# Performance work log

Hardware: AMD Instinct MI355X
Metric: run time of the kernel (lower is better)

## Reference

```python
import jax, jax.numpy as jnp
import numpy as np

K = 1024
D = 64
BETA = 0.25
DECAY = 0.99
EPS = 1e-05


def setup_inputs() -> dict:
    key = jax.random.key(0)
    k1, k2 = jax.random.split(key)
    z = jax.random.normal(k1, (32, D, 64, 64), dtype=jnp.float32)
    # nn.init.uniform_(weight, -1/K, 1/K)
    embedding = jax.random.uniform(k2, (K, D), dtype=jnp.float32, minval=-1.0 / K, maxval=1.0 / K)
    # post-_maybe_init_ema_from_embedding state
    cluster_size = jnp.ones((K,), dtype=jnp.float32)
    embed_avg = embedding.copy()
    return {"z": z, "embedding": embedding, "cluster_size": cluster_size, "embed_avg": embed_avg}


def reference(z, embedding, cluster_size, embed_avg):
    B, C, H, W = z.shape
    z_nhwc = jnp.transpose(z, (0, 2, 3, 1))            # [B,H,W,D]
    flat = z_nhwc.reshape(-1, D)                        # [N,D]

    x2 = jnp.sum(flat * flat, axis=1, keepdims=True)    # [N,1]
    w2 = jnp.sum(embedding * embedding, axis=1)         # [K]
    dist = x2 + w2[None, :] - 2.0 * flat @ embedding.T  # [N,K]
    idx = jnp.argmin(dist, axis=1)                      # [N] int

    z_q = embedding[idx].reshape(z_nhwc.shape)          # gather

    # EMA codebook update (training, update=True)
    counts = jax.ops.segment_sum(jnp.ones_like(idx, dtype=jnp.float32), idx, num_segments=K)
    embed_sum = jax.ops.segment_sum(flat, idx, num_segments=K)  # [K,D]
    new_cluster_size = cluster_size * DECAY + (1.0 - DECAY) * counts
    new_embed_avg = embed_avg * DECAY + (1.0 - DECAY) * embed_sum
    n = jnp.sum(new_cluster_size)
    smoothed = (new_cluster_size + EPS) / (n + K * EPS) * n
    new_embedding = new_embed_avg / smoothed[:, None]

    # commitment loss (z_q detached) + straight-through estimator
    loss = BETA * jnp.mean((z_nhwc - jax.lax.stop_gradient(z_q)) ** 2)
    z_q_ste = z_nhwc + jax.lax.stop_gradient(z_q - z_nhwc)
    z_q_out = jnp.transpose(z_q_ste, (0, 3, 1, 2))      # back to [B,C,H,W]
    return (z_q_out, idx, loss, new_embedding, new_cluster_size, new_embed_avg)
```

## Files before the change

kernel.cpp:

```cpp
#include <hip/hip_runtime.h>
#include <hip/hip_bf16.h>

#define NROWS 131072
#define DDIM  64
#define KCODES 1024
#define HW    4096

#define OFF_ZQ   0ull
#define OFF_IDX  8388608ull
#define OFF_LOSS 8519680ull
#define OFF_EMB  8519681ull
#define OFF_NCS  8585217ull
#define OFF_EAVG 8586241ull

#define SCR_B0    34078724ull
#define SCR_WLO   (SCR_B0 + 131072ull)
#define SCR_W2O   (SCR_B0 + 262144ull)
#define LCAP      20480u

#define FWS_KSCR   16777216ull
#define FWS_ES     16777216ull
#define FWS_CNTF   17039360ull
#define FWS_SX2    17043456ull
#define FWS_SMOOTH 17047552ull
#define FWS_LIST   17301504ull
#define FWS_RMIN   17383424ull
#define FWS_CNTR   17547264ull
#define FWS_TOTAL  17547268ull

#define WSO_KSCR   262144ull
#define WSO_LOSSB  786432ull
#define WSO_SMOOTH 788480ull
#define WSO_CNT    792576ull
#define WSO_ESUM   858112ull

#define GAPTHR 8e-5f

typedef __attribute__((ext_vector_type(8))) short bf16x8;
typedef __attribute__((ext_vector_type(4))) float f32x4;

#define GLOAD_LDS16(gp, lp)                                                     \
    __builtin_amdgcn_global_load_lds(                                           \
        (const __attribute__((address_space(1))) void*)(gp),                    \
        (__attribute__((address_space(3))) void*)(lp), 16, 0, 0)

__device__ __forceinline__ float np_sumsq64(const float* v) {
#pragma clang fp contract(off)
    float r0 = v[0]*v[0], r1 = v[1]*v[1], r2 = v[2]*v[2], r3 = v[3]*v[3];
    float r4 = v[4]*v[4], r5 = v[5]*v[5], r6 = v[6]*v[6], r7 = v[7]*v[7];
    for (int i = 8; i < 64; i += 8) {
        r0 += v[i+0]*v[i+0]; r1 += v[i+1]*v[i+1];
        r2 += v[i+2]*v[i+2]; r3 += v[i+3]*v[i+3];
        r4 += v[i+4]*v[i+4]; r5 += v[i+5]*v[i+5];
        r6 += v[i+6]*v[i+6]; r7 += v[i+7]*v[i+7];
    }
    return ((r0+r1)+(r2+r3))+((r4+r5)+(r6+r7));
}
__device__ __forceinline__ float mul_rn(float a, float b) {
#pragma clang fp contract(off)
    return a * b;
}
__device__ __forceinline__ float add_rn(float a, float b) {
#pragma clang fp contract(off)
    return a + b;
}
__device__ __forceinline__ float sub2_rn(float s, float a) {
#pragma clang fp contract(off)
    return s - 2.0f * a;
}
__device__ __forceinline__ unsigned bf16rne(float v) {
    unsigned b = __float_as_uint(v);
    return (b + 0x7FFFu + ((b >> 16) & 1u)) >> 16;
}
__device__ __forceinline__ float bfu2f(unsigned short u) {
    return __uint_as_float(((unsigned)u) << 16);
}
__device__ __forceinline__ unsigned flipf(float v) {
    unsigned b = __float_as_uint(v);
    return b ^ (0x80000000u | (unsigned)((int)b >> 31));
}
__device__ __forceinline__ float unflip_val(unsigned u) {
    u &= 0xFFFFFC00u;
    unsigned mask = 0x80000000u | (unsigned)((int)(~u) >> 31);
    return __uint_as_float(u ^ mask);
}

__global__ __launch_bounds__(256) void prep_kernel(
        const float* __restrict__ emb, unsigned short* __restrict__ wh,
        unsigned short* __restrict__ wl, float* __restrict__ w2,
        float* __restrict__ embT) {
    __shared__ float tile[64][65];
    const int t = threadIdx.x;
    const int kb = blockIdx.x * 64;
#pragma unroll
    for (int i = 0; i < 16; ++i) {
        const int e = t + i * 256;
        const int kl = e >> 6, d = e & 63;
        const float v = emb[(size_t)(kb + kl) * DDIM + d];
        tile[kl][d] = v;
        const unsigned rh = bf16rne(v);
        const float lv = v - bfu2f((unsigned short)rh);
        wh[(size_t)(kb + kl) * DDIM + d] = (unsigned short)rh;
        wl[(size_t)(kb + kl) * DDIM + d] = (unsigned short)bf16rne(lv);
    }
    __syncthreads();
    if (t < 64) w2[kb + t] = np_sumsq64(&tile[t][0]);
#pragma unroll
    for (int i = 0; i < 16; ++i) {
        const int e = t + i * 256;
        const int d = e >> 6, kl = e & 63;
        embT[(size_t)d * KCODES + kb + kl] = tile[kl][d];
    }
}

#define CBLOAD(S, c)                                                          \
    { const size_t a_ = ((size_t)(((c) * 16 + col) * DDIM + grp * 8));        \
      wh##S##0 = *(const bf16x8*)(wh + a_);                                   \
      wh##S##1 = *(const bf16x8*)(wh + a_ + 32);                              \
      wl##S##0 = *(const bf16x8*)(wl + a_);                                   \
      wl##S##1 = *(const bf16x8*)(wl + a_ + 32); }

__global__ __launch_bounds__(512, 2) void score2_kernel(
        const float* __restrict__ z, const float* __restrict__ emb,
        const unsigned short* __restrict__ wh, const unsigned short* __restrict__ wl,
        const float* __restrict__ w2g, float* __restrict__ out,
        unsigned short* __restrict__ xT, unsigned* __restrict__ list,
        unsigned long long* __restrict__ rmin, unsigned* __restrict__ counter) {
    __shared__ __attribute__((aligned(16))) unsigned short sxt[64][512];
    __shared__ __attribute__((aligned(16))) unsigned short cb[2][2][4][512];
    __shared__ unsigned k1s[512];

    const int tid = threadIdx.x;
    const int lane = tid & 63, wid = tid >> 6;
    const int col = lane & 15, grp = lane >> 4;
    const int nb = blockIdx.x * 512;
    const int b = nb >> 12, hb = (nb >> 6) & 63;
    const int w4 = (tid & 15) * 4, h8 = (tid >> 4) & 7, dg = tid >> 7;

    {
#pragma unroll
        for (int j = 0; j < 16; ++j) {
            const int d = dg * 16 + j;
            const float4 v = *(const float4*)&z[((size_t)(b * 64 + d)) * HW + (hb + h8) * 64 + w4];
            ushort4 u;
            u.x = (unsigned short)bf16rne(v.x);
            u.y = (unsigned short)bf16rne(v.y);
            u.z = (unsigned short)bf16rne(v.z);
            u.w = (unsigned short)bf16rne(v.w);
            *(ushort4*)&sxt[d][h8 * 64 + w4] = u;
        }
    }
    __syncthreads();

    bf16x8 fx[4][2];
#pragma unroll
    for (int rt = 0; rt < 4; ++rt)
#pragma unroll
        for (int kh = 0; kh < 2; ++kh) {
            const int row = wid * 64 + rt * 16 + col;
            bf16x8 f;
#pragma unroll
            for (int j = 0; j < 8; ++j)
                f[j] = (short)sxt[kh * 32 + grp * 8 + j][row];
            fx[rt][kh] = f;
            *(bf16x8*)&xT[(size_t)(nb + row) * DDIM + kh * 32 + grp * 8] = f;
        }

    const int pr = wid >> 2, sW = (wid >> 1) & 1, khW = wid & 1;
    const unsigned short* gsrc = (pr ? wl : wh) + khW * 32 + grp * 8
                               + (size_t)(sW * 16 + col) * DDIM;

    GLOAD_LDS16(gsrc, &cb[0][pr][sW * 2 + khW][0]);
    asm volatile("s_waitcnt vmcnt(0)" ::: "memory");
    __builtin_amdgcn_s_barrier();

    unsigned m1[4] = {~0u, ~0u, ~0u, ~0u}, m2[4] = {~0u, ~0u, ~0u, ~0u};

    for (int rd = 0; rd < 32; ++rd) {
        const int cur = rd & 1;
        if (rd < 31)
            GLOAD_LDS16(gsrc + (size_t)(rd + 1) * 32 * DDIM,
                        &cb[cur ^ 1][pr][sW * 2 + khW][0]);
#pragma unroll
        for (int s = 0; s < 2; ++s) {
            const bf16x8 vh0 = *(const bf16x8*)&cb[cur][0][s * 2 + 0][lane * 8];
            const bf16x8 vh1 = *(const bf16x8*)&cb[cur][0][s * 2 + 1][lane * 8];
            const bf16x8 vl0 = *(const bf16x8*)&cb[cur][1][s * 2 + 0][lane * 8];
            const bf16x8 vl1 = *(const bf16x8*)&cb[cur][1][s * 2 + 1][lane * 8];
            const int c = rd * 2 + s;
            const float4 w2v = *(const float4*)&w2g[c * 16 + grp * 4];
            const float* w2p = (const float*)&w2v;
#pragma unroll
            for (int rt = 0; rt < 4; ++rt) {
                f32x4 aA = {0.f, 0.f, 0.f, 0.f}, aB = {0.f, 0.f, 0.f, 0.f};
                aA = __builtin_amdgcn_mfma_f32_16x16x32_bf16(vh0, fx[rt][0], aA, 0, 0, 0);
                aA = __builtin_amdgcn_mfma_f32_16x16x32_bf16(vl0, fx[rt][0], aA, 0, 0, 0);
                aB = __builtin_amdgcn_mfma_f32_16x16x32_bf16(vh1, fx[rt][1], aB, 0, 0, 0);
                aB = __builtin_amdgcn_mfma_f32_16x16x32_bf16(vl1, fx[rt][1], aB, 0, 0, 0);
#pragma unroll
                for (int r = 0; r < 4; ++r) {
                    const float val = fmaf(-2.f, aA[r] + aB[r], w2p[r]);
                    const unsigned u = (flipf(val) & 0xFFFFFC00u) |
                                       (unsigned)(c * 16 + grp * 4 + r);
                    const unsigned mx = m1[rt] > u ? m1[rt] : u;
                    m1[rt] = m1[rt] < u ? m1[rt] : u;
                    m2[rt] = m2[rt] < mx ? m2[rt] : mx;
                }
            }
        }
        asm volatile("s_waitcnt vmcnt(0) lgkmcnt(0)" ::: "memory");
        __builtin_amdgcn_s_barrier();
    }

#pragma unroll
    for (int rt = 0; rt < 4; ++rt) {
        for (int off = 16; off <= 32; off <<= 1) {
            const unsigned o1 = (unsigned)__shfl_xor((int)m1[rt], off, 64);
            const unsigned o2 = (unsigned)__shfl_xor((int)m2[rt], off, 64);
            const unsigned mx = m1[rt] > o1 ? m1[rt] : o1;
            m1[rt] = m1[rt] < o1 ? m1[rt] : o1;
            const unsigned t2 = m2[rt] < o2 ? m2[rt] : o2;
            m2[rt] = t2 < mx ? t2 : mx;
        }
    }

    bool flag[4];
    unsigned long long mrt[4];
    unsigned wavecnt = 0;
#pragma unroll
    for (int rt = 0; rt < 4; ++rt) {
        flag[rt] = (grp == 0) &&
                   ((unflip_val(m2[rt]) - unflip_val(m1[rt])) < GAPTHR);
        mrt[rt] = __ballot(flag[rt]);
        wavecnt += (unsigned)__popcll(mrt[rt]);
    }

    if (grp == 0) {
#pragma unroll
        for (int rt = 0; rt < 4; ++rt) {
            const unsigned k = m1[rt] & 1023u;
            out[OFF_IDX + (size_t)(nb + wid * 64 + rt * 16 + col)] = (float)k;
            k1s[wid * 64 + rt * 16 + col] = k;
        }
    }

    unsigned base = 0;
    if (lane == 0 && wavecnt) base = atomicAdd(counter, wavecnt);
    base = (unsigned)__shfl((int)base, 0, 64);
    unsigned offrt = 0;
#pragma unroll
    for (int rt = 0; rt < 4; ++rt) {
        if (flag[rt]) {
            const unsigned offin =
                (unsigned)__popcll(mrt[rt] & ((lane == 0) ? 0ull : (~0ull >> (64 - lane))));
            const unsigned slot = base + offrt + offin;
            if (slot < LCAP) {
                list[slot] = (unsigned)(nb + wid * 64 + rt * 16 + col);
                rmin[slot] = ~0ull;
            }
        }
        offrt += (unsigned)__popcll(mrt[rt]);
    }

    __syncthreads();
    {
        const int r0 = h8 * 64 + w4;
        const float* e0 = emb + (size_t)k1s[r0 + 0] * DDIM;
        const float* e1 = emb + (size_t)k1s[r0 + 1] * DDIM;
        const float* e2 = emb + (size_t)k1s[r0 + 2] * DDIM;
        const float* e3 = emb + (size_t)k1s[r0 + 3] * DDIM;
#pragma unroll
        for (int j = 0; j < 16; ++j) {
            const int d = dg * 16 + j;
            float4 q;
            q.x = e0[d]; q.y = e1[d]; q.z = e2[d]; q.w = e3[d];
            *(float4*)&out[((size_t)(b * 64 + d)) * HW + (hb + h8) * 64 + w4] = q;
        }
    }
}

__global__ __launch_bounds__(256, 1) void rescanb_kernel(
        const float* __restrict__ z, const float* __restrict__ emb,
        const float* __restrict__ w2, const unsigned* __restrict__ list,
        const unsigned* __restrict__ counter,
        unsigned long long* __restrict__ rmin) {
    const int lane = threadIdx.x & 63;
    const int wid = __builtin_amdgcn_readfirstlane(threadIdx.x >> 6);
    unsigned cnt = __builtin_amdgcn_readfirstlane(*counter);
    if (cnt > LCAP) cnt = LCAP;
    if (cnt == 0) return;
    const unsigned W = ((cnt + 63) >> 6) * 8;

    for (unsigned w = blockIdx.x * 4 + wid; w < W; w += gridDim.x * 4) {
        const unsigned g = w >> 3, p = w & 7;
        const unsigned slot = g * 64 + lane;
        const bool valid = slot < cnt;
        const unsigned n = list[valid ? slot : 0];
        const unsigned hw = n & 4095u, bb = n >> 12;

        float x[64];
#pragma unroll
        for (int d = 0; d < 64; ++d)
            x[d] = z[(size_t)(bb * 64 + d) * (size_t)HW + hw];

        float r[8];
#pragma unroll
        for (int j = 0; j < 8; ++j) r[j] = mul_rn(x[j], x[j]);
#pragma unroll
        for (int i = 8; i < 64; i += 8)
#pragma unroll
            for (int j = 0; j < 8; ++j)
                r[j] = add_rn(r[j], mul_rn(x[i + j], x[i + j]));
        const float x2 = add_rn(add_rn(add_rn(r[0], r[1]), add_rn(r[2], r[3])),
                                add_rn(add_rn(r[4], r[5]), add_rn(r[6], r[7])));

        unsigned long long best = ~0ull;
        const int k0 = (int)p * 128;
        for (int k = k0; k < k0 + 128; k += 2) {
            const float* wa = emb + (size_t)k * DDIM;
            const float* wb = wa + DDIM;
            float aa = 0.f, ab = 0.f;
#pragma unroll
            for (int d = 0; d < 64; ++d) {
                aa = fmaf(x[d], wa[d], aa);
                ab = fmaf(x[d], wb[d], ab);
            }
            const float da = sub2_rn(add_rn(x2, w2[k]),     aa);
            const float db = sub2_rn(add_rn(x2, w2[k + 1]), ab);
            const unsigned long long ua =
                ((unsigned long long)flipf(da) << 10) | (unsigned long long)k;
            const unsigned long long ub =
                ((unsigned long long)flipf(db) << 10) | (unsigned long long)(k + 1);
            best = best < ua ? best : ua;
            best = best < ub ? best : ub;
        }
        if (valid) atomicMin(&rmin[slot], best);
    }
}

__global__ __launch_bounds__(256) void fix_kernel(
        const unsigned* __restrict__ list, const unsigned long long* __restrict__ rmin,
        const unsigned* __restrict__ counter, const float* __restrict__ emb,
        float* __restrict__ out) {
    unsigned cnt = *counter;
    if (cnt > LCAP) cnt = LCAP;
    const int lane = threadIdx.x & 63, ws = threadIdx.x >> 6;
    const unsigned t = blockIdx.x * 4 + ws;
    if (t >= cnt) return;
    const unsigned long long u = rmin[t];
    if (u == ~0ull) return;
    const unsigned k = (unsigned)(u & 1023ull);
    const unsigned n = list[t];
    if (lane == 0) out[OFF_IDX + (size_t)n] = (float)k;
    const unsigned hw = n & 4095u, bb = n >> 12;
    out[((size_t)(bb * 64 + lane)) * HW + hw] = emb[(size_t)k * DDIM + lane];
}

__global__ __launch_bounds__(256) void gather_kernel(
        const float* __restrict__ idxf, const unsigned short* __restrict__ xT,
        float* __restrict__ es, float* __restrict__ cntf, float* __restrict__ sx2a) {
    const int k = blockIdx.x;
    const int lane = threadIdx.x & 63, wid = threadIdx.x >> 6;
    const float fk = (float)k;
    float acc = 0.f, s2 = 0.f;
    unsigned cnt = 0;
    const int wbase = wid * 32768;

    float4 cur = *(const float4*)&idxf[wbase + lane * 4];
    for (int it = 0; it < 128; ++it) {
        float4 nxt;
        if (it + 1 < 128)
            nxt = *(const float4*)&idxf[wbase + (it + 1) * 256 + lane * 4];
        const float* cp = (const float*)&cur;
#pragma unroll
        for (int j = 0; j < 4; ++j) {
            unsigned long long m = __ballot(cp[j] == fk);
            cnt += (unsigned)__popcll(m);
            while (m) {
                const int src = __ffsll(m) - 1;
                m &= m - 1;
                const int n = wbase + it * 256 + src * 4 + j;
                const float xv = bfu2f(xT[(size_t)n * DDIM + lane]);
                acc += xv;
                s2 = fmaf(xv, xv, s2);
            }
        }
        cur = nxt;
    }
#pragma unroll
    for (int off = 32; off > 0; off >>= 1) s2 += __shfl_down(s2, off, 64);
    __shared__ float sacc[4][64];
    __shared__ float ssx2[4];
    __shared__ unsigned scnt[4];
    sacc[wid][lane] = acc;
    if (lane == 0) { ssx2[wid] = s2; scnt[wid] = cnt; }
    __syncthreads();
    if (wid == 0) {
        const float t = sacc[0][lane] + sacc[1][lane] + sacc[2][lane] + sacc[3][lane];
        es[(size_t)k * DDIM + lane] = t;
        if (lane == 0) {
            cntf[k] = (float)(scnt[0] + scnt[1] + scnt[2] + scnt[3]);
            sx2a[k] = ssx2[0] + ssx2[1] + ssx2[2] + ssx2[3];
        }
    }
}

__global__ __launch_bounds__(1024) void fin1_f(
        const float* __restrict__ cs, const float* __restrict__ emb,
        float* __restrict__ out, const float* __restrict__ w2,
        const float* __restrict__ es, const float* __restrict__ cntf,
        const float* __restrict__ sx2a, float* __restrict__ smoothed) {
    const int k = threadIdx.x;
    const float cnt = cntf[k];
    const float w2k = w2[k];
    const float* ek = es + (size_t)k * DDIM;
    const float* wk = emb + (size_t)k * DDIM;
    float dt = 0.f;
#pragma unroll
    for (int d = 0; d < DDIM; ++d) dt = fmaf(ek[d], wk[d], dt);
    const float lp = sx2a[k] - 2.f * dt + cnt * w2k;
    const float ncs = fmaf(0.01f, cnt, 0.99f * cs[k]);

    __shared__ float red[1024];
    red[k] = ncs;
    __syncthreads();
    for (int s = 512; s > 0; s >>= 1) {
        if (k < s) red[k] += red[k + s];
        __syncthreads();
    }
    const float nn = red[0];
    __syncthreads();
    red[k] = lp;
    __syncthreads();
    for (int s = 512; s > 0; s >>= 1) {
        if (k < s) red[k] += red[k + s];
        __syncthreads();
    }
    smoothed[k] = (ncs + 1e-5f) / (nn + 1024.f * 1e-5f) * nn;
    out[OFF_NCS + (size_t)k] = ncs;
    if (k == 0) out[OFF_LOSS] = 0.25f * red[0] / 8388608.f;
}

__global__ __launch_bounds__(256) void fin2_f(
        const float* __restrict__ eavg, float* __restrict__ out,
        const float* __restrict__ es, const float* __restrict__ smoothed) {
    const int e = blockIdx.x * 256 + threadIdx.x;
    const float ea = fmaf(0.01f, es[e], 0.99f * eavg[e]);
    out[OFF_EAVG + (size_t)e] = ea;
    out[OFF_EMB  + (size_t)e] = ea / smoothed[e >> 6];
}


#define CBCOMP(S, c)                                                          \
    { const float4 w2v = *(const float4*)&w2s[(c) * 16 + grp * 4];            \
      const float* w2p = (const float*)&w2v;                                  \
      _Pragma("unroll")                                                       \
      for (int rt = 0; rt < 2; ++rt) {                                        \
        f32x4 aA = {0.f,0.f,0.f,0.f}, aB = {0.f,0.f,0.f,0.f};                 \
        aA = __builtin_amdgcn_mfma_f32_16x16x32_bf16(wh##S##0, fx[rt][0], aA, 0, 0, 0); \
        aA = __builtin_amdgcn_mfma_f32_16x16x32_bf16(wl##S##0, fx[rt][0], aA, 0, 0, 0); \
        aB = __builtin_amdgcn_mfma_f32_16x16x32_bf16(wh##S##1, fx[rt][1], aB, 0, 0, 0); \
        aB = __builtin_amdgcn_mfma_f32_16x16x32_bf16(wl##S##1, fx[rt][1], aB, 0, 0, 0); \
        _Pragma("unroll")                                                     \
        for (int r = 0; r < 4; ++r) {                                         \
          const float val = fmaf(-2.f, aA[r] + aB[r], w2p[r]);                \
          const unsigned u = (flipf(val) & 0xFFFFFC00u) |                     \
                             (unsigned)((c) * 16 + grp * 4 + r);              \
          const unsigned mx = m1[rt] > u ? m1[rt] : u;                        \
          m1[rt] = m1[rt] < u ? m1[rt] : u;                                   \
          m2[rt] = m2[rt] < mx ? m2[rt] : mx;                                 \
        } } }

__global__ __launch_bounds__(512, 4) void score_kernel(
        const float* __restrict__ z,
        const unsigned short* __restrict__ wh, const unsigned short* __restrict__ wl,
        const float* __restrict__ w2, unsigned* __restrict__ kscr) {
    __shared__ __attribute__((aligned(16))) unsigned short sxt[64][260];
    __shared__ float w2s[KCODES];

    const int tid = threadIdx.x;
    const int lane = tid & 63, wid = tid >> 6;
    const int col = lane & 15, grp = lane >> 4;
    const int nb = blockIdx.x * 256;
    const int b = nb >> 12, hb = (nb >> 6) & 63;

    for (int i = tid; i < KCODES; i += 512) w2s[i] = w2[i];
    {
        const int h = lane >> 4, w4 = (lane & 15) * 4;
        const int row = h * 64 + w4;
#pragma unroll
        for (int it = 0; it < 8; ++it) {
            const int d = wid + 8 * it;
            const float4 v = *(const float4*)&z[((size_t)(b * 64 + d)) * HW + (hb + h) * 64 + w4];
            ushort4 u;
            u.x = (unsigned short)bf16rne(v.x);
            u.y = (unsigned short)bf16rne(v.y);
            u.z = (unsigned short)bf16rne(v.z);
            u.w = (unsigned short)bf16rne(v.w);
            *(ushort4*)&sxt[d][row] = u;
        }
    }
    __syncthreads();

    bf16x8 fx[2][2];
#pragma unroll
    for (int rt = 0; rt < 2; ++rt)
#pragma unroll
        for (int kh = 0; kh < 2; ++kh) {
            const int row = wid * 32 + rt * 16 + col;
            bf16x8 f;
#pragma unroll
            for (int j = 0; j < 8; ++j)
                f[j] = (short)sxt[kh * 32 + grp * 8 + j][row];
            fx[rt][kh] = f;
        }

    unsigned m1[2] = {~0u, ~0u}, m2[2] = {~0u, ~0u};
    bf16x8 whA0, whA1, wlA0, wlA1, whB0, whB1, wlB0, wlB1;

    CBLOAD(A, 0)
    for (int c = 0; c < 64; c += 2) {
        CBLOAD(B, c + 1)
        CBCOMP(A, c)
        if (c + 2 < 64) CBLOAD(A, c + 2)
        CBCOMP(B, c + 1)
    }
#pragma unroll
    for (int rt = 0; rt < 2; ++rt) {
        for (int off = 16; off <= 32; off <<= 1) {
            const unsigned o1 = (unsigned)__shfl_xor((int)m1[rt], off, 64);
            const unsigned o2 = (unsigned)__shfl_xor((int)m2[rt], off, 64);
            const unsigned mx = m1[rt] > o1 ? m1[rt] : o1;
            m1[rt] = m1[rt] < o1 ? m1[rt] : o1;
            const unsigned t2 = m2[rt] < o2 ? m2[rt] : o2;
            m2[rt] = t2 < mx ? t2 : mx;
        }
        if (grp == 0) {
            const bool fl = (unflip_val(m2[rt]) - unflip_val(m1[rt])) < GAPTHR;
            kscr[nb + wid * 32 + rt * 16 + col] =
                (m1[rt] & 1023u) | (fl ? 0x80000000u : 0u);
        }
    }
}

__global__ __launch_bounds__(512, 4) void output_kernel(
        const float* __restrict__ z, const float* __restrict__ emb,
        const float* __restrict__ embT, const float* __restrict__ w2,
        float* __restrict__ out, const unsigned* __restrict__ kscr,
        float* __restrict__ esum_p, unsigned* __restrict__ cnt_p,
        float* __restrict__ lossb, int pmask) {
    __shared__ __attribute__((aligned(16))) unsigned short sxt[64][260];
    __shared__ unsigned k1s[256];
    __shared__ float redl[8];

    const int tid = threadIdx.x;
    const int lane = tid & 63, wid = tid >> 6;
    const int nb = blockIdx.x * 256;
    const int b = nb >> 12, hb = (nb >> 6) & 63;

    {
        const int h = lane >> 4, w4 = (lane & 15) * 4;
        const int row = h * 64 + w4;
#pragma unroll
        for (int it = 0; it < 8; ++it) {
            const int d = wid + 8 * it;
            const float4 v = *(const float4*)&z[((size_t)(b * 64 + d)) * HW + (hb + h) * 64 + w4];
            ushort4 u;
            u.x = (unsigned short)bf16rne(v.x);
            u.y = (unsigned short)bf16rne(v.y);
            u.z = (unsigned short)bf16rne(v.z);
            u.w = (unsigned short)bf16rne(v.w);
            *(ushort4*)&sxt[d][row] = u;
        }
    }

    unsigned kf = 0;
    if (lane < 32) kf = kscr[nb + wid * 32 + lane];
    int k1 = (int)(kf & 1023u);
    unsigned long long need = __ballot((lane < 32) && (kf & 0x80000000u));
    while (need) {
        const int src = __ffsll(need) - 1;
        need &= need - 1;
        const int nr = nb + wid * 32 + src;
        const int wq = nr & 63, hq = (nr >> 6) & 63, bq = nr >> 12;
        const float xv = z[(size_t)bq * DDIM * HW + (size_t)lane * HW + hq * 64 + wq];
        const float p = mul_rn(xv, xv);
        float r = 0.f;
        for (int i = 0; i < 8; ++i) {
            const float t = __shfl(p, (i << 3) + (lane & 7), 64);
            r = add_rn(r, t);
        }
        const float s01 = add_rn(r, __shfl_xor(r, 1, 64));
        const float s03 = add_rn(s01, __shfl_xor(s01, 2, 64));
        const float s07 = add_rn(s03, __shfl_xor(s03, 4, 64));
        const float x2s = __shfl(s07, 0, 64);

        float acc[16];
#pragma unroll
        for (int j = 0; j < 16; ++j) acc[j] = 0.f;
        for (int d = 0; d < DDIM; ++d) {
            const float xd = __shfl(xv, d, 64);
            const float* ecol = embT + (size_t)d * KCODES + lane;
#pragma unroll
            for (int j = 0; j < 16; ++j)
                acc[j] = fmaf(ecol[64 * j], xd, acc[j]);
        }
        float bv = 1e30f;
        int bk = KCODES;
#pragma unroll
        for (int j = 0; j < 16; ++j) {
            const int kk = lane + 64 * j;
            const float s  = add_rn(x2s, w2[kk]);
            const float dv = sub2_rn(s, acc[j]);
            if (dv < bv) { bv = dv; bk = kk; }
        }
        for (int off = 32; off > 0; off >>= 1) {
            const float ov = __shfl_xor(bv, off, 64);
            const int   ok = __shfl_xor(bk, off, 64);
            if (ov < bv || (ov == bv && ok < bk)) { bv = ov; bk = ok; }
        }
        if (lane == src) k1 = bk;
    }
    if (lane < 32) k1s[wid * 32 + lane] = (unsigned)k1;
    __syncthreads();

    const int part = blockIdx.x & pmask;
    if (tid < 256) {
        const unsigned myk = k1s[tid];
        out[OFF_IDX + (size_t)(nb + tid)] = (float)myk;
        atomicAdd(&cnt_p[part * KCODES + myk], 1u);
    }

    float ls = 0.f;
    {
        const int h = lane >> 4, w4 = (lane & 15) * 4;
        const int row = h * 64 + w4;
#pragma unroll 2
        for (int it = 0; it < 8; ++it) {
            const int d = wid + 8 * it;
            float4 q;
            float* qp = (float*)&q;
#pragma unroll
            for (int j = 0; j < 4; ++j) {
                const unsigned k = k1s[row + j];
                const float wv = emb[(size_t)k * DDIM + d];
                qp[j] = wv;
                const float diff = bfu2f(sxt[d][row + j]) - wv;
                ls = fmaf(diff, diff, ls);
            }
            *(float4*)&out[((size_t)(b * 64 + d)) * HW + (hb + h) * 64 + w4] = q;
        }
    }
#pragma unroll
    for (int off = 32; off > 0; off >>= 1) ls += __shfl_down(ls, off, 64);
    if (lane == 0) redl[wid] = ls;
    __syncthreads();
    if (tid == 0) {
        float t = 0.f;
#pragma unroll
        for (int i = 0; i < 8; ++i) t += redl[i];
        lossb[blockIdx.x] = t;
    }
    {
        float* ep = esum_p + (size_t)part * 65536;
        for (int r = 0; r < 32; ++r) {
            const int row = wid * 32 + r;
            atomicAdd(&ep[(size_t)k1s[row] * DDIM + lane], bfu2f(sxt[lane][row]));
        }
    }
}

__global__ __launch_bounds__(1024) void finalize1_kernel(
        const float* __restrict__ cs, float* __restrict__ out,
        const unsigned* __restrict__ cnt_p, const float* __restrict__ lossb,
        float* __restrict__ smoothed, int P) {
    const int k = threadIdx.x;
    unsigned c = 0;
    for (int p = 0; p < P; ++p) c += cnt_p[p * KCODES + k];
    const float ncs = fmaf(0.01f, (float)c, 0.99f * cs[k]);

    __shared__ float red[1024];
    red[k] = ncs;
    __syncthreads();
    for (int s = 512; s > 0; s >>= 1) {
        if (k < s) red[k] += red[k + s];
        __syncthreads();
    }
    const float nn = red[0];
    smoothed[k] = (ncs + 1e-5f) / (nn + 1024.f * 1e-5f) * nn;
    out[OFF_NCS + (size_t)k] = ncs;

    __syncthreads();
    red[k] = (k < 512) ? lossb[k] : 0.f;
    __syncthreads();
    for (int s = 512; s > 0; s >>= 1) {
        if (k < s) red[k] += red[k + s];
        __syncthreads();
    }
    if (k == 0) out[OFF_LOSS] = 0.25f * red[0] / 8388608.f;
}

__global__ __launch_bounds__(256) void finalize2_kernel(
        const float* __restrict__ eavg, float* __restrict__ out,
        const float* __restrict__ esum_p, const float* __restrict__ smoothed,
        int P) {
    const int e = blockIdx.x * 256 + threadIdx.x;
    float s = 0.f;
    for (int p = 0; p < P; ++p) s += esum_p[(size_t)p * 65536 + e];
    const float ea = fmaf(0.01f, s, 0.99f * eavg[e]);
    out[OFF_EAVG + (size_t)e] = ea;
    out[OFF_EMB  + (size_t)e] = ea / smoothed[e >> 6];
}


extern "C" void kernel_launch(void* const* d_in, const int* in_sizes, int n_in,
                              void* d_out, int out_size, void* d_ws, size_t ws_size,
                              hipStream_t stream) {
    const float* z    = (const float*)d_in[0];
    const float* emb  = (const float*)d_in[1];
    const float* cs   = (const float*)d_in[2];
    const float* eavg = (const float*)d_in[3];
    float* out = (float*)d_out;

    unsigned short* wh = (unsigned short*)((char*)d_out + SCR_B0);
    unsigned short* wl = (unsigned short*)((char*)d_out + SCR_WLO);
    float*          w2 = (float*)((char*)d_out + SCR_W2O);
    char* ws = (char*)d_ws;

    if (ws_size >= FWS_TOTAL) {
        unsigned short*     xT   = (unsigned short*)ws;
        float*              es   = (float*)(ws + FWS_ES);
        float*              cntf = (float*)(ws + FWS_CNTF);
        float*              sx2a = (float*)(ws + FWS_SX2);
        float*              smoo = (float*)(ws + FWS_SMOOTH);
        unsigned*           list = (unsigned*)(ws + FWS_LIST);
        unsigned long long* rmin = (unsigned long long*)(ws + FWS_RMIN);
        unsigned*           cntr = (unsigned*)(ws + FWS_CNTR);
        float*              embT = (float*)(ws + FWS_KSCR);

        (void)hipMemsetAsync(cntr, 0, 4, stream);
        prep_kernel<<<16, 256, 0, stream>>>(emb, wh, wl, w2, embT);
        score2_kernel<<<NROWS / 512, 512, 0, stream>>>(
            z, emb, wh, wl, w2, out, xT, list, rmin, cntr);
        rescanb_kernel<<<256, 256, 0, stream>>>(z, emb, w2, list, cntr, rmin);
        fix_kernel<<<LCAP / 4, 256, 0, stream>>>(list, rmin, cntr, emb, out);
        gather_kernel<<<KCODES, 256, 0, stream>>>(out + OFF_IDX, xT, es, cntf, sx2a);
        fin1_f<<<1, 1024, 0, stream>>>(cs, emb, out, w2, es, cntf, sx2a, smoo);
        fin2_f<<<256, 256, 0, stream>>>(eavg, out, es, smoo);
    } else {
        int P = 1;
        for (int p = 16; p >= 1; p >>= 1)
            if (ws_size >= WSO_ESUM + (size_t)p * 262144ull) { P = p; break; }

        float*    embT   = (float*)ws;
        unsigned* kscr   = (unsigned*)(ws + WSO_KSCR);
        float*    lossb  = (float*)(ws + WSO_LOSSB);
        float*    smooth = (float*)(ws + WSO_SMOOTH);
        unsigned* cnt_p  = (unsigned*)(ws + WSO_CNT);
        float*    esum_p = (float*)(ws + WSO_ESUM);

        (void)hipMemsetAsync(ws + WSO_CNT, 0, 65536 + (size_t)P * 262144ull, stream);
        prep_kernel<<<16, 256, 0, stream>>>(emb, wh, wl, w2, embT);
        score_kernel<<<NROWS / 256, 512, 0, stream>>>(z, wh, wl, w2, kscr);
        output_kernel<<<NROWS / 256, 512, 0, stream>>>(
            z, emb, embT, w2, out, kscr, esum_p, cnt_p, lossb, P - 1);
        finalize1_kernel<<<1, 1024, 0, stream>>>(cs, out, cnt_p, lossb, smooth, P);
        finalize2_kernel<<<256, 256, 0, stream>>>(eavg, out, esum_p, smooth, P);
    }
}
```

Baseline: 298.3 us.

## Fuse EMA finalize into gather kernel and stage w2 in LDS

Merges the gather, finalize-1 and finalize-2 kernels into one per-code kernel. The global normalizer n is computed analytically from the sum of cluster_size precomputed in prep, and the loss is accumulated atomically and then scaled by a tiny final kernel. The score kernel also caches w2 in shared memory and chains all four MFMAs into one accumulator. This removes a single-block reduction kernel and two launches, at the cost of atomic float-summation nondeterminism and a serial MFMA dependency chain.

```diff
diff --git a/kernel.cpp b/kernel.cpp
--- a/kernel.cpp
+++ b/kernel.cpp
@@ -23,10 +23,12 @@
 #define FWS_CNTF   17039360ull
 #define FWS_SX2    17043456ull
 #define FWS_SMOOTH 17047552ull
+#define FWS_SCS    17047556ull
 #define FWS_LIST   17301504ull
 #define FWS_RMIN   17383424ull
 #define FWS_CNTR   17547264ull
-#define FWS_TOTAL  17547268ull
+#define FWS_LOSSA  17547268ull
+#define FWS_TOTAL  17547272ull
 
 #define WSO_KSCR   262144ull
 #define WSO_LOSSB  786432ull
@@ -86,10 +88,12 @@
 }
 
 __global__ __launch_bounds__(256) void prep_kernel(
-        const float* __restrict__ emb, unsigned short* __restrict__ wh,
-        unsigned short* __restrict__ wl, float* __restrict__ w2,
-        float* __restrict__ embT) {
+        const float* __restrict__ emb, const float* __restrict__ cs,
+        unsigned short* __restrict__ wh, unsigned short* __restrict__ wl,
+        float* __restrict__ w2, float* __restrict__ embT,
+        float* __restrict__ scs) {
     __shared__ float tile[64][65];
+    __shared__ float sred[4];
     const int t = threadIdx.x;
     const int kb = blockIdx.x * 64;
 #pragma unroll
@@ -111,6 +115,14 @@
         const int d = e >> 6, kl = e & 63;
         embT[(size_t)d * KCODES + kb + kl] = tile[kl][d];
     }
+    if (blockIdx.x == 0) {
+        float v = cs[t * 4] + cs[t * 4 + 1] + cs[t * 4 + 2] + cs[t * 4 + 3];
+#pragma unroll
+        for (int off = 32; off > 0; off >>= 1) v += __shfl_down(v, off, 64);
+        if ((t & 63) == 0) sred[t >> 6] = v;
+        __syncthreads();
+        if (t == 0) scs[0] = sred[0] + sred[1] + sred[2] + sred[3];
+    }
 }
 
 #define CBLOAD(S, c)                                                          \
@@ -128,6 +140,7 @@
         unsigned long long* __restrict__ rmin, unsigned* __restrict__ counter) {
     __shared__ __attribute__((aligned(16))) unsigned short sxt[64][512];
     __shared__ __attribute__((aligned(16))) unsigned short cb[2][2][4][512];
+    __shared__ float w2s[KCODES];
     __shared__ unsigned k1s[512];
 
     const int tid = threadIdx.x;
@@ -136,6 +149,8 @@
     const int nb = blockIdx.x * 512;
     const int b = nb >> 12, hb = (nb >> 6) & 63;
     const int w4 = (tid & 15) * 4, h8 = (tid >> 4) & 7, dg = tid >> 7;
+
+    for (int i = tid; i < KCODES; i += 512) w2s[i] = w2g[i];
 
     {
 #pragma unroll
@@ -188,18 +203,18 @@
             const bf16x8 vl0 = *(const bf16x8*)&cb[cur][1][s * 2 + 0][lane * 8];
             const bf16x8 vl1 = *(const bf16x8*)&cb[cur][1][s * 2 + 1][lane * 8];
             const int c = rd * 2 + s;
-            const float4 w2v = *(const float4*)&w2g[c * 16 + grp * 4];
+            const float4 w2v = *(const float4*)&w2s[c * 16 + grp * 4];
             const float* w2p = (const float*)&w2v;
 #pragma unroll
             for (int rt = 0; rt < 4; ++rt) {
-                f32x4 aA = {0.f, 0.f, 0.f, 0.f}, aB = {0.f, 0.f, 0.f, 0.f};
-                aA = __builtin_amdgcn_mfma_f32_16x16x32_bf16(vh0, fx[rt][0], aA, 0, 0, 0);
-                aA = __builtin_amdgcn_mfma_f32_16x16x32_bf16(vl0, fx[rt][0], aA, 0, 0, 0);
-                aB = __builtin_amdgcn_mfma_f32_16x16x32_bf16(vh1, fx[rt][1], aB, 0, 0, 0);
-                aB = __builtin_amdgcn_mfma_f32_16x16x32_bf16(vl1, fx[rt][1], aB, 0, 0, 0);
+                f32x4 a = {0.f, 0.f, 0.f, 0.f};
+                a = __builtin_amdgcn_mfma_f32_16x16x32_bf16(vh0, fx[rt][0], a, 0, 0, 0);
+                a = __builtin_amdgcn_mfma_f32_16x16x32_bf16(vl0, fx[rt][0], a, 0, 0, 0);
+                a = __builtin_amdgcn_mfma_f32_16x16x32_bf16(vh1, fx[rt][1], a, 0, 0, 0);
+                a = __builtin_amdgcn_mfma_f32_16x16x32_bf16(vl1, fx[rt][1], a, 0, 0, 0);
 #pragma unroll
                 for (int r = 0; r < 4; ++r) {
-                    const float val = fmaf(-2.f, aA[r] + aB[r], w2p[r]);
+                    const float val = fmaf(-2.f, a[r], w2p[r]);
                     const unsigned u = (flipf(val) & 0xFFFFFC00u) |
                                        (unsigned)(c * 16 + grp * 4 + r);
                     const unsigned mx = m1[rt] > u ? m1[rt] : u;
@@ -356,9 +371,12 @@
     out[((size_t)(bb * 64 + lane)) * HW + hw] = emb[(size_t)k * DDIM + lane];
 }
 
-__global__ __launch_bounds__(256) void gather_kernel(
+__global__ __launch_bounds__(256) void gatherfin_kernel(
         const float* __restrict__ idxf, const unsigned short* __restrict__ xT,
-        float* __restrict__ es, float* __restrict__ cntf, float* __restrict__ sx2a) {
+        const float* __restrict__ emb, const float* __restrict__ cs,
+        const float* __restrict__ eavg, const float* __restrict__ w2,
+        const float* __restrict__ scs, float* __restrict__ out,
+        float* __restrict__ lossA) {
     const int k = blockIdx.x;
     const int lane = threadIdx.x & 63, wid = threadIdx.x >> 6;
     const float fk = (float)k;
@@ -396,58 +414,34 @@
     if (lane == 0) { ssx2[wid] = s2; scnt[wid] = cnt; }
     __syncthreads();
     if (wid == 0) {
-        const float t = sacc[0][lane] + sacc[1][lane] + sacc[2][lane] + sacc[3][lane];
-        es[(size_t)k * DDIM + lane] = t;
+        const float es = sacc[0][lane] + sacc[1][lane] + sacc[2][lane] + sacc[3][lane];
+        const float cntk = (float)(scnt[0] + scnt[1] + scnt[2] + scnt[3]);
+        const float sx2 = ssx2[0] + ssx2[1] + ssx2[2] + ssx2[3];
+        const float w2k = w2[k];
+        const float wkd = emb[(size_t)k * DDIM + lane];
+
+        float dt = es * wkd;
+#pragma unroll
+        for (int off = 32; off > 0; off >>= 1) dt += __shfl_down(dt, off, 64);
+
+        const float ncs = fmaf(0.01f, cntk, 0.99f * cs[k]);
+        const float nn  = fmaf(0.99f, scs[0], 1310.72f);
+        const float smoothed = (ncs + 1e-5f) / (nn + 1024.f * 1e-5f) * nn;
+
         if (lane == 0) {
-            cntf[k] = (float)(scnt[0] + scnt[1] + scnt[2] + scnt[3]);
-            sx2a[k] = ssx2[0] + ssx2[1] + ssx2[2] + ssx2[3];
-        }
-    }
-}
-
-__global__ __launch_bounds__(1024) void fin1_f(
-        const float* __restrict__ cs, const float* __restrict__ emb,
-        float* __restrict__ out, const float* __restrict__ w2,
-        const float* __restrict__ es, const float* __restrict__ cntf,
-        const float* __restrict__ sx2a, float* __restrict__ smoothed) {
-    const int k = threadIdx.x;
-    const float cnt = cntf[k];
-    const float w2k = w2[k];
-    const float* ek = es + (size_t)k * DDIM;
-    const float* wk = emb + (size_t)k * DDIM;
-    float dt = 0.f;
-#pragma unroll
-    for (int d = 0; d < DDIM; ++d) dt = fmaf(ek[d], wk[d], dt);
-    const float lp = sx2a[k] - 2.f * dt + cnt * w2k;
-    const float ncs = fmaf(0.01f, cnt, 0.99f * cs[k]);
-
-    __shared__ float red[1024];
-    red[k] = ncs;
-    __syncthreads();
-    for (int s = 512; s > 0; s >>= 1) {
-        if (k < s) red[k] += red[k + s];
-        __syncthreads();
-    }
-    const float nn = red[0];
-    __syncthreads();
-    red[k] = lp;
-    __syncthreads();
-    for (int s = 512; s > 0; s >>= 1) {
-        if (k < s) red[k] += red[k + s];
-        __syncthreads();
-    }
-    smoothed[k] = (ncs + 1e-5f) / (nn + 1024.f * 1e-5f) * nn;
-    out[OFF_NCS + (size_t)k] = ncs;
-    if (k == 0) out[OFF_LOSS] = 0.25f * red[0] / 8388608.f;
-}
-
-__global__ __launch_bounds__(256) void fin2_f(
-        const float* __restrict__ eavg, float* __restrict__ out,
-        const float* __restrict__ es, const float* __restrict__ smoothed) {
-    const int e = blockIdx.x * 256 + threadIdx.x;
-    const float ea = fmaf(0.01f, es[e], 0.99f * eavg[e]);
-    out[OFF_EAVG + (size_t)e] = ea;
-    out[OFF_EMB  + (size_t)e] = ea / smoothed[e >> 6];
+            out[OFF_NCS + (size_t)k] = ncs;
+            atomicAdd(lossA, sx2 - 2.f * dt + cntk * w2k);
+        }
+        const float ea = fmaf(0.01f, es, 0.99f * eavg[(size_t)k * DDIM + lane]);
+        out[OFF_EAVG + (size_t)k * DDIM + lane] = ea;
+        out[OFF_EMB  + (size_t)k * DDIM + lane] = ea / smoothed;
+    }
+}
+
+__global__ __launch_bounds__(64) void lossfin_kernel(
+        const float* __restrict__ lossA, float* __restrict__ out) {
+    if (threadIdx.x == 0)
+        out[OFF_LOSS] = 0.25f * lossA[0] / 8388608.f;
 }
 
 
@@ -729,24 +723,22 @@
 
     if (ws_size >= FWS_TOTAL) {
         unsigned short*     xT   = (unsigned short*)ws;
-        float*              es   = (float*)(ws + FWS_ES);
-        float*              cntf = (float*)(ws + FWS_CNTF);
-        float*              sx2a = (float*)(ws + FWS_SX2);
-        float*              smoo = (float*)(ws + FWS_SMOOTH);
+        float*              scs  = (float*)(ws + FWS_SCS);
         unsigned*           list = (unsigned*)(ws + FWS_LIST);
         unsigned long long* rmin = (unsigned long long*)(ws + FWS_RMIN);
         unsigned*           cntr = (unsigned*)(ws + FWS_CNTR);
+        float*              lossA = (float*)(ws + FWS_LOSSA);
         float*              embT = (float*)(ws + FWS_KSCR);
 
-        (void)hipMemsetAsync(cntr, 0, 4, stream);
-        prep_kernel<<<16, 256, 0, stream>>>(emb, wh, wl, w2, embT);
+        (void)hipMemsetAsync(ws + FWS_CNTR, 0, 8, stream);
+        prep_kernel<<<16, 256, 0, stream>>>(emb, cs, wh, wl, w2, embT, scs);
         score2_kernel<<<NROWS / 512, 512, 0, stream>>>(
             z, emb, wh, wl, w2, out, xT, list, rmin, cntr);
         rescanb_kernel<<<256, 256, 0, stream>>>(z, emb, w2, list, cntr, rmin);
         fix_kernel<<<LCAP / 4, 256, 0, stream>>>(list, rmin, cntr, emb, out);
-        gather_kernel<<<KCODES, 256, 0, stream>>>(out + OFF_IDX, xT, es, cntf, sx2a);
-        fin1_f<<<1, 1024, 0, stream>>>(cs, emb, out, w2, es, cntf, sx2a, smoo);
-        fin2_f<<<256, 256, 0, stream>>>(eavg, out, es, smoo);
+        gatherfin_kernel<<<KCODES, 256, 0, stream>>>(
+            out + OFF_IDX, xT, emb, cs, eavg, w2, scs, out, lossA);
+        lossfin_kernel<<<1, 64, 0, stream>>>(lossA, out);
     } else {
         int P = 1;
         for (int p = 16; p >= 1; p >>= 1)
@@ -760,7 +752,8 @@
         float*    esum_p = (float*)(ws + WSO_ESUM);
 
         (void)hipMemsetAsync(ws + WSO_CNT, 0, 65536 + (size_t)P * 262144ull, stream);
-        prep_kernel<<<16, 256, 0, stream>>>(emb, wh, wl, w2, embT);
+        prep_kernel<<<16, 256, 0, stream>>>(emb, cs, wh, wl, w2, embT,
+                                            (float*)(ws + WSO_SMOOTH));
         score_kernel<<<NROWS / 256, 512, 0, stream>>>(z, wh, wl, w2, kscr);
         output_kernel<<<NROWS / 256, 512, 0, stream>>>(
             z, emb, embT, w2, out, kscr, esum_p, cnt_p, lossb, P - 1);
```

Measured after the change: 275.9 us. 1.08x faster.
